# Performance work log

Measured on AMD Instinct MI355X. Metric: run time of the kernel, lower is better.

Reference implementation:

```python
import jax, jax.numpy as jnp
import numpy as np

M, N = 4096, 4096

def _make_expk(n):
    k = np.arange(n, dtype=np.float64) * np.pi / (2.0 * n)
    return jnp.asarray(np.stack([np.cos(k), np.sin(k)], axis=-1), dtype=jnp.float32)

def setup_inputs() -> dict:
    key = jax.random.key(0)
    x = jax.random.normal(key, (M, N), dtype=jnp.float32)
    return {"x": x, "expkM": _make_expk(M), "expkN": _make_expk(N)}

def _idct_last(X, expk):
    """1D IDCT (inverse of unnormalized DCT-II) along last axis via Makhoul's
    N-point FFT trick. expk[k] = (cos, sin) of pi*k/(2N), i.e. e^{j pi k/(2N)}."""
    n = X.shape[-1]
    Xv = X * 0.5
    # V[k] = (Xv[k] - j*Xv[n-k]) * e^{j pi k/(2n)}, with imag part 0 at k=0
    tail = -jnp.flip(Xv, axis=-1)[..., :-1]
    Vi = jnp.concatenate([jnp.zeros_like(Xv[..., :1]), tail], axis=-1)
    W = expk[:, 0] + 1j * expk[:, 1]
    V = (Xv + 1j * Vi) * W
    v = jnp.fft.ifft(V, axis=-1).real.astype(X.dtype)
    # de-interleave: out[2m] = v[m], out[2m+1] = v[n-1-m]
    out = jnp.zeros_like(X)
    out = out.at[..., 0::2].set(v[..., : n - n // 2])
    out = out.at[..., 1::2].set(jnp.flip(v, axis=-1)[..., : n // 2])
    return out

def reference(x, expkM, expkN):
    # separable 2D IDCT: last axis (N) then first axis (M)
    y = _idct_last(x, expkN)
    y = _idct_last(y.T, expkM).T
    return y
```

## Files before the change

### kernel.cpp

```cpp
#include <hip/hip_runtime.h>
#include <math.h>


#define TT 256

constexpr float W64R[32] = {
    1.0f, 0.995184726672197f, 0.980785280403230f, 0.956940335732209f,
    0.923879532511287f, 0.881921264348355f, 0.831469612302545f, 0.773010453362737f,
    0.707106781186548f, 0.634393284163645f, 0.555570233019602f, 0.471396736825998f,
    0.382683432365090f, 0.290284677254462f, 0.195090322016128f, 0.0980171403295606f,
    0.0f, -0.0980171403295606f, -0.195090322016128f, -0.290284677254462f,
    -0.382683432365090f, -0.471396736825998f, -0.555570233019602f, -0.634393284163645f,
    -0.707106781186548f, -0.773010453362737f, -0.831469612302545f, -0.881921264348355f,
    -0.923879532511287f, -0.956940335732209f, -0.980785280403230f, -0.995184726672197f};
constexpr float W64I[32] = {
    0.0f, 0.0980171403295606f, 0.195090322016128f, 0.290284677254462f,
    0.382683432365090f, 0.471396736825998f, 0.555570233019602f, 0.634393284163645f,
    0.707106781186548f, 0.773010453362737f, 0.831469612302545f, 0.881921264348355f,
    0.923879532511287f, 0.956940335732209f, 0.980785280403230f, 0.995184726672197f,
    1.0f, 0.995184726672197f, 0.980785280403230f, 0.956940335732209f,
    0.923879532511287f, 0.881921264348355f, 0.831469612302545f, 0.773010453362737f,
    0.707106781186548f, 0.634393284163645f, 0.555570233019602f, 0.471396736825998f,
    0.382683432365090f, 0.290284677254462f, 0.195090322016128f, 0.0980171403295606f};

__device__ __forceinline__ constexpr int brev(int x, int bits) {
    int r = 0;
    for (int i = 0; i < bits; ++i) { r = (r << 1) | (x & 1); x >>= 1; }
    return r;
}

__device__ __forceinline__ float vadd(float a, float b) { return a + b; }
__device__ __forceinline__ float vsub(float a, float b) { return a - b; }
__device__ __forceinline__ float vmul(float a, float s) { return a * s; }

template <int NP, typename V>
__device__ __forceinline__ void fft_dif(V* re, V* im) {
#pragma unroll
    for (int h = NP / 2; h >= 1; h >>= 1) {
#pragma unroll
        for (int b = 0; b < NP; b += 2 * h) {
#pragma unroll
            for (int k = 0; k < h; ++k) {
                V ur = re[b + k], ui = im[b + k];
                V vr = re[b + k + h], vi = im[b + k + h];
                V dr = vsub(ur, vr), di = vsub(ui, vi);
                re[b + k] = vadd(ur, vr);
                im[b + k] = vadd(ui, vi);
                float wr = W64R[k * (32 / h)], wi = W64I[k * (32 / h)];
                re[b + k + h] = vsub(vmul(dr, wr), vmul(di, wi));
                im[b + k + h] = vadd(vmul(dr, wi), vmul(di, wr));
            }
        }
    }
}

__global__ void tw_init_kernel(float2* __restrict__ tw2048,
                               float2* __restrict__ ca, float2* __restrict__ cb,
                               float2* __restrict__ cc, float2* __restrict__ cd,
                               float4* __restrict__ cAC) {
    int k = blockIdx.x * TT + threadIdx.x;
    const double s = 0.5 / 4096.0;
    double aw = M_PI * (double)k / 2048.0;
    double wr = cos(aw), wi = sin(aw);
    double a1 = M_PI * (double)k / 8192.0;
    double e1r = cos(a1), e1i = sin(a1);
    double a2 = M_PI * (double)(k + 2048) / 8192.0;
    double e2r = cos(a2), e2i = sin(a2);
    double Ar = s * ((1.0 - wi) * e1r - wr * e1i);
    double Ai = s * ((1.0 - wi) * e1i + wr * e1r);
    double Br = (k == 0) ? 0.0 : Ai;
    double Bi = (k == 0) ? 0.0 : -Ar;
    double Cr = s * ((1.0 + wi) * e2r + wr * e2i);
    double Ci = s * ((1.0 + wi) * e2i - wr * e2r);
    ca[k] = make_float2((float)Ar, (float)Ai);
    cb[k] = make_float2((float)Br, (float)Bi);
    cc[k] = make_float2((float)Cr, (float)Ci);
    cd[k] = make_float2((float)Ci, (float)-Cr);
    cAC[k] = make_float4((float)Ar, (float)Ai, (float)Cr, (float)Ci);
    double at = M_PI * (double)k / 1024.0;
    tw2048[k] = make_float2((float)cos(at), (float)sin(at));
}

__global__ __launch_bounds__(TT) void col_a_kernel(
    const float* __restrict__ x, const float4* __restrict__ cAC,
    const float2* __restrict__ tw2048, float2* __restrict__ T1) {
    const int l = threadIdx.x;
    const int par = l >> 5;
    const int c = blockIdx.x * 32 + (l & 31);
    const int k1 = blockIdx.y * 4 + threadIdx.y;
    float fr[16], fi[16];
#pragma unroll
    for (int a = 0; a < 16; ++a) {
        int k2 = 2 * a + par;
        int k = k1 + 64 * k2;
        float xa = x[(size_t)k * 4096 + c];
        float xb = x[(size_t)((4096 - k) & 4095) * 4096 + c];
        float xc = x[(size_t)(2048 + k) * 4096 + c];
        float xd = x[(size_t)(2048 - k) * 4096 + c];
        float4 P = cAC[k];
        float bs = (k == 0) ? 0.0f : 1.0f;
        fr[a] = P.x * xa + bs * P.y * xb + P.z * xc + P.w * xd;
        fi[a] = P.y * xa - bs * P.x * xb + P.w * xc - P.z * xd;
    }
    fft_dif<16, float>(fr, fi);
    const float sgn = par ? -1.0f : 1.0f;
#pragma unroll
    for (int j = 0; j < 16; ++j) {
        int n = brev(j, 4);
        float wr = par ? W64R[2 * n] : 1.0f;
        float wi = par ? W64I[2 * n] : 0.0f;
        float vr = fr[j] * wr - fi[j] * wi;
        float vi = fr[j] * wi + fi[j] * wr;
        float orr = __shfl_xor(vr, 32, 64);
        float oii = __shfl_xor(vi, 32, 64);
        float zr = orr + sgn * vr;
        float zi = oii + sgn * vi;
        int n2 = par ? (n + 16) : n;
        float2 w2 = tw2048[k1 * n2];
        float2 o = make_float2(zr * w2.x - zi * w2.y,
                               zr * w2.y + zi * w2.x);
        T1[(size_t)(k1 * 32 + n2) * 4096 + c] = o;
    }
}

__global__ __launch_bounds__(TT, 1) void col_b_kernel(
    const float2* __restrict__ T1, float* __restrict__ out) {
    const int t = threadIdx.x;
    const int wv = t >> 6;
    const int l = t & 63;
    const int par = l >> 5;
    const int c = blockIdx.x * 32 + (l & 31);
    const int n2 = blockIdx.y * 4 + wv;
    float fr[32], fi[32];
#pragma unroll
    for (int a = 0; a < 32; ++a) {
        int k1 = 2 * a + par;
        float2 v = T1[(size_t)(k1 * 32 + n2) * 4096 + c];
        fr[a] = v.x; fi[a] = v.y;
    }
    fft_dif<32, float>(fr, fi);
    const float sgn = par ? -1.0f : 1.0f;
#pragma unroll
    for (int j = 0; j < 32; ++j) {
        int n = brev(j, 5);
        float wr = par ? W64R[n] : 1.0f;
        float wi = par ? W64I[n] : 0.0f;
        float vr = fr[j] * wr - fi[j] * wi;
        float vi = fr[j] * wi + fi[j] * wr;
        float orr = __shfl_xor(vr, 32, 64);
        float oii = __shfl_xor(vi, 32, 64);
        float zr = orr + sgn * vr;
        float zi = oii + sgn * vi;
        int n1 = par ? (n + 32) : n;
        int m = 32 * n1 + n2;
        int r_re = (n1 < 32) ? 4 * m     : 8191 - 4 * m;
        int r_im = (n1 < 32) ? 4 * m + 2 : 8189 - 4 * m;
        out[(size_t)r_re * 4096 + c] = zr;
        out[(size_t)r_im * 4096 + c] = zi;
    }
}

#define C_SQ2 0.70710678118654752440f
__device__ __forceinline__ void radix8(const float* ar, const float* ai,
                                       float* tr, float* ti) {
    float s04r = ar[0] + ar[4], s04i = ai[0] + ai[4];
    float d04r = ar[0] - ar[4], d04i = ai[0] - ai[4];
    float s26r = ar[2] + ar[6], s26i = ai[2] + ai[6];
    float d26r = ar[2] - ar[6], d26i = ai[2] - ai[6];
    float E0r = s04r + s26r, E0i = s04i + s26i;
    float E1r = d04r - d26i, E1i = d04i + d26r;
    float E2r = s04r - s26r, E2i = s04i - s26i;
    float E3r = d04r + d26i, E3i = d04i - d26r;
    float s15r = ar[1] + ar[5], s15i = ai[1] + ai[5];
    float d15r = ar[1] - ar[5], d15i = ai[1] - ai[5];
    float s37r = ar[3] + ar[7], s37i = ai[3] + ai[7];
    float d37r = ar[3] - ar[7], d37i = ai[3] - ai[7];
    float O0r = s15r + s37r, O0i = s15i + s37i;
    float O1r = d15r - d37i, O1i = d15i + d37r;
    float O2r = s15r - s37r, O2i = s15i - s37i;
    float O3r = d15r + d37i, O3i = d15i - d37r;
    float W1r = C_SQ2 * (O1r - O1i), W1i = C_SQ2 * (O1r + O1i);
    float W2r = -O2i, W2i = O2r;
    float W3r = -C_SQ2 * (O3r + O3i), W3i = C_SQ2 * (O3r - O3i);
    tr[0] = E0r + O0r; ti[0] = E0i + O0i;
    tr[4] = E0r - O0r; ti[4] = E0i - O0i;
    tr[1] = E1r + W1r; ti[1] = E1i + W1i;
    tr[5] = E1r - W1r; ti[5] = E1i - W1i;
    tr[2] = E2r + W2r; ti[2] = E2i + W2i;
    tr[6] = E2r - W2r; ti[6] = E2i - W2i;
    tr[3] = E3r + W3r; ti[3] = E3i + W3i;
    tr[7] = E3r - W3r; ti[7] = E3i - W3i;
}

__global__ __launch_bounds__(TT) void idct_rows_kernel(
    const float2* __restrict__ ca, const float2* __restrict__ cb,
    const float2* __restrict__ cc, const float2* __restrict__ cd,
    const float2* __restrict__ tw2048, float* __restrict__ io) {
    __shared__ float pool[8576];
    float* b0r = pool;
    float* b0i = pool + 2112;
    float* b1r = pool + 4224;
    float* b1i = pool + 6400;
    float* stg = pool + 4224;
    const int t = threadIdx.x;
    float* __restrict__ xr = io + (size_t)blockIdx.x * 4096;

#pragma unroll
    for (int u = 0; u < 4; ++u) {
        int idx = t + 256 * u;
        float4 v = ((const float4*)xr)[idx];
        *(float4*)&stg[4 * idx] = v;
    }
    __syncthreads();

    float zr[8], zi[8], tr[8], ti[8];
#pragma unroll
    for (int p = 0; p < 8; ++p) {
        int k = t + 256 * p;
        float xa = stg[k];
        float xb = stg[(4096 - k) & 4095];
        float xc = stg[2048 + k];
        float xd = stg[2048 - k];
        float2 A = ca[k], B = cb[k], C = cc[k], D = cd[k];
        zr[p] = A.x * xa + B.x * xb + C.x * xc + D.x * xd;
        zi[p] = A.y * xa + B.y * xb + C.y * xc + D.y * xd;
    }
    radix8(zr, zi, tr, ti);
    {
        int baseA = 8 * t + (t >> 2);
        b0r[baseA] = tr[0]; b0i[baseA] = ti[0];
#pragma unroll
        for (int q = 1; q < 8; ++q) {
            float2 w = tw2048[(t * q) & 2047];
            b0r[baseA + q] = w.x * tr[q] - w.y * ti[q];
            b0i[baseA + q] = w.x * ti[q] + w.y * tr[q];
        }
    }
    __syncthreads();
    {
        float ar[8], ai[8];
        int rb = t + (t >> 5);
#pragma unroll
        for (int p = 0; p < 8; ++p) { ar[p] = b0r[rb + 264 * p]; ai[p] = b0i[rb + 264 * p]; }
        radix8(ar, ai, tr, ti);
        int j = t >> 3, k = t & 7, wj = 8 * j;
        int baseB = 68 * j + k;
        b1r[baseB] = tr[0]; b1i[baseB] = ti[0];
#pragma unroll
        for (int q = 1; q < 8; ++q) {
            int off = baseB + 8 * q + (q >> 1);
            float2 w = tw2048[(wj * q) & 2047];
            b1r[off] = w.x * tr[q] - w.y * ti[q];
            b1i[off] = w.x * ti[q] + w.y * tr[q];
        }
    }
    __syncthreads();
    {
        float ar[8], ai[8];
        int rb = t + (t >> 4);
#pragma unroll
        for (int p = 0; p < 8; ++p) { ar[p] = b1r[rb + 272 * p]; ai[p] = b1i[rb + 272 * p]; }
        radix8(ar, ai, tr, ti);
        int j = t >> 6, wj = 64 * j, k = t & 63;
        int baseC = 528 * j + k + (k >> 5);
        b0r[baseC] = tr[0]; b0i[baseC] = ti[0];
#pragma unroll
        for (int q = 1; q < 8; ++q) {
            int off = baseC + 66 * q;
            float2 w = tw2048[(wj * q) & 2047];
            b0r[off] = w.x * tr[q] - w.y * ti[q];
            b0i[off] = w.x * ti[q] + w.y * tr[q];
        }
    }
    __syncthreads();
#pragma unroll
    for (int u = 0; u < 2; ++u) {
        int b = t + 256 * u;
        int rb = b + (b >> 5);
        int wb = b + (b >> 4);
        float a0r = b0r[rb], a0i = b0i[rb];
        float a1r = b0r[rb + 528], a1i = b0i[rb + 528];
        float a2r = b0r[rb + 1056], a2i = b0i[rb + 1056];
        float a3r = b0r[rb + 1584], a3i = b0i[rb + 1584];
        float s02r = a0r + a2r, s02i = a0i + a2i;
        float d02r = a0r - a2r, d02i = a0i - a2i;
        float s13r = a1r + a3r, s13i = a1i + a3i;
        float d13r = a1r - a3r, d13i = a1i - a3i;
        b1r[wb] = s02r + s13r;          b1i[wb] = s02i + s13i;
        b1r[wb + 544] = d02r - d13i;    b1i[wb + 544] = d02i + d13r;
        b1r[wb + 1088] = s02r - s13r;   b1i[wb + 1088] = s02i - s13i;
        b1r[wb + 1632] = d02r + d13i;   b1i[wb + 1632] = d02i - d13r;
    }
    __syncthreads();
#pragma unroll
    for (int i = 0; i < 4; ++i) {
        int s = t + 256 * i;
        int l2 = 2047 - s;
        int ms = s + (s >> 4);
        int ml = l2 + (l2 >> 4);
        float4 o = make_float4(b1r[ms], b1i[ml], b1i[ms], b1r[ml]);
        *(float4*)&xr[4 * s] = o;
    }
}

extern "C" void kernel_launch(void* const* d_in, const int* in_sizes, int n_in,
                              void* d_out, int out_size, void* d_ws, size_t ws_size,
                              hipStream_t stream) {
    const float* x = (const float*)d_in[0];
    float* out = (float*)d_out;

    float2* tw2048 = (float2*)d_ws;
    float2* ca = (float2*)((char*)d_ws + 1 * 16384);
    float2* cb = (float2*)((char*)d_ws + 2 * 16384);
    float2* cc = (float2*)((char*)d_ws + 3 * 16384);
    float2* cd = (float2*)((char*)d_ws + 4 * 16384);
    float4* cAC = (float4*)((char*)d_ws + 5 * 16384);
    float2* T1 = (float2*)((char*)d_ws + (1 << 20));

    tw_init_kernel<<<8, TT, 0, stream>>>(tw2048, ca, cb, cc, cd, cAC);
    col_a_kernel<<<dim3(128, 16), dim3(64, 4), 0, stream>>>(x, cAC, tw2048, T1);
    col_b_kernel<<<dim3(128, 8), TT, 0, stream>>>(T1, out);
    idct_rows_kernel<<<4096, TT, 0, stream>>>(ca, cb, cc, cd, tw2048, out);
}
```

Measured before the change: 188.4 us.

## Stage column-pass input through LDS with direct global-to-LDS 16-byte loads

```diff
diff --git a/kernel.cpp b/kernel.cpp
--- a/kernel.cpp
+++ b/kernel.cpp
@@ -81,27 +81,54 @@
     tw2048[k] = make_float2((float)cos(at), (float)sin(at));
 }
 
-__global__ __launch_bounds__(TT) void col_a_kernel(
+typedef __attribute__((address_space(1))) const unsigned int* ga_u32;
+typedef __attribute__((address_space(3))) unsigned int* la_u32;
+
+__global__ __launch_bounds__(128) void col_a_kernel(
     const float* __restrict__ x, const float4* __restrict__ cAC,
     const float2* __restrict__ tw2048, float2* __restrict__ T1) {
+    __shared__ float L[2][4096];
     const int l = threadIdx.x;
+    const int ty = threadIdx.y;
     const int par = l >> 5;
-    const int c = blockIdx.x * 32 + (l & 31);
-    const int k1 = blockIdx.y * 4 + threadIdx.y;
+    const int cb = blockIdx.x * 32;
+    const int c = cb + (l & 31);
+    const int k1 = blockIdx.y * 2 + ty;
+
+    const int rg = l >> 3;
+    const int cq = (l & 7) * 4;
+#pragma unroll
+    for (int i = 0; i < 16; ++i) {
+        int j = 8 * i + rg;
+        int k2 = j >> 2, s = j & 3;
+        int kk = k1 + 64 * k2;
+        int row = (s == 0) ? kk
+                : (s == 1) ? ((4096 - kk) & 4095)
+                : (s == 2) ? (2048 + kk)
+                           : (2048 - kk);
+        __builtin_amdgcn_global_load_lds(
+            (ga_u32)(const void*)(x + (size_t)row * 4096 + cb + cq),
+            (la_u32)(void*)&L[ty][i * 256 + 4 * l], 16, 0, 0);
+    }
+    __builtin_amdgcn_sched_barrier(0);
+    asm volatile("s_waitcnt vmcnt(0)" ::: "memory");
+    __builtin_amdgcn_sched_barrier(0);
+
     float fr[16], fi[16];
 #pragma unroll
     for (int a = 0; a < 16; ++a) {
-        int k2 = 2 * a + par;
-        int k = k1 + 64 * k2;
-        float xa = x[(size_t)k * 4096 + c];
-        float xb = x[(size_t)((4096 - k) & 4095) * 4096 + c];
-        float xc = x[(size_t)(2048 + k) * 4096 + c];
-        float xd = x[(size_t)(2048 - k) * 4096 + c];
+        int base = (8 * a + 4 * par) * 32 + (l & 31);
+        float xa = L[ty][base];
+        float xb = L[ty][base + 32];
+        float xc = L[ty][base + 64];
+        float xd = L[ty][base + 96];
+        int k = k1 + 64 * (2 * a + par);
         float4 P = cAC[k];
         float bs = (k == 0) ? 0.0f : 1.0f;
         fr[a] = P.x * xa + bs * P.y * xb + P.z * xc + P.w * xd;
         fi[a] = P.y * xa - bs * P.x * xb + P.w * xc - P.z * xd;
     }
+
     fft_dif<16, float>(fr, fi);
     const float sgn = par ? -1.0f : 1.0f;
 #pragma unroll
@@ -318,7 +345,7 @@
     float2* T1 = (float2*)((char*)d_ws + (1 << 20));
 
     tw_init_kernel<<<8, TT, 0, stream>>>(tw2048, ca, cb, cc, cd, cAC);
-    col_a_kernel<<<dim3(128, 16), dim3(64, 4), 0, stream>>>(x, cAC, tw2048, T1);
+    col_a_kernel<<<dim3(128, 32), dim3(64, 2), 0, stream>>>(x, cAC, tw2048, T1);
     col_b_kernel<<<dim3(128, 8), TT, 0, stream>>>(T1, out);
     idct_rows_kernel<<<4096, TT, 0, stream>>>(ca, cb, cc, cd, tw2048, out);
 }
```

After: 190.3 us. No clear change (+1.0%).

## Fuse all IDCT stages into one persistent cooperative kernel with grid syncs

Applied to the files above, without the earlier changes.

```diff
diff --git a/kernel.cpp b/kernel.cpp
--- a/kernel.cpp
+++ b/kernel.cpp
@@ -1,5 +1,8 @@
 #include <hip/hip_runtime.h>
+#include <hip/hip_cooperative_groups.h>
 #include <math.h>
+
+namespace cg = cooperative_groups;
 
 
 #define TT 256
@@ -29,134 +32,24 @@
     return r;
 }
 
-__device__ __forceinline__ float vadd(float a, float b) { return a + b; }
-__device__ __forceinline__ float vsub(float a, float b) { return a - b; }
-__device__ __forceinline__ float vmul(float a, float s) { return a * s; }
-
-template <int NP, typename V>
-__device__ __forceinline__ void fft_dif(V* re, V* im) {
+template <int NP>
+__device__ __forceinline__ void fft_dif(float* re, float* im) {
 #pragma unroll
     for (int h = NP / 2; h >= 1; h >>= 1) {
 #pragma unroll
         for (int b = 0; b < NP; b += 2 * h) {
 #pragma unroll
             for (int k = 0; k < h; ++k) {
-                V ur = re[b + k], ui = im[b + k];
-                V vr = re[b + k + h], vi = im[b + k + h];
-                V dr = vsub(ur, vr), di = vsub(ui, vi);
-                re[b + k] = vadd(ur, vr);
-                im[b + k] = vadd(ui, vi);
+                float ur = re[b + k], ui = im[b + k];
+                float vr = re[b + k + h], vi = im[b + k + h];
+                float dr = ur - vr, di = ui - vi;
+                re[b + k] = ur + vr;
+                im[b + k] = ui + vi;
                 float wr = W64R[k * (32 / h)], wi = W64I[k * (32 / h)];
-                re[b + k + h] = vsub(vmul(dr, wr), vmul(di, wi));
-                im[b + k + h] = vadd(vmul(dr, wi), vmul(di, wr));
-            }
-        }
-    }
-}
-
-__global__ void tw_init_kernel(float2* __restrict__ tw2048,
-                               float2* __restrict__ ca, float2* __restrict__ cb,
-                               float2* __restrict__ cc, float2* __restrict__ cd,
-                               float4* __restrict__ cAC) {
-    int k = blockIdx.x * TT + threadIdx.x;
-    const double s = 0.5 / 4096.0;
-    double aw = M_PI * (double)k / 2048.0;
-    double wr = cos(aw), wi = sin(aw);
-    double a1 = M_PI * (double)k / 8192.0;
-    double e1r = cos(a1), e1i = sin(a1);
-    double a2 = M_PI * (double)(k + 2048) / 8192.0;
-    double e2r = cos(a2), e2i = sin(a2);
-    double Ar = s * ((1.0 - wi) * e1r - wr * e1i);
-    double Ai = s * ((1.0 - wi) * e1i + wr * e1r);
-    double Br = (k == 0) ? 0.0 : Ai;
-    double Bi = (k == 0) ? 0.0 : -Ar;
-    double Cr = s * ((1.0 + wi) * e2r + wr * e2i);
-    double Ci = s * ((1.0 + wi) * e2i - wr * e2r);
-    ca[k] = make_float2((float)Ar, (float)Ai);
-    cb[k] = make_float2((float)Br, (float)Bi);
-    cc[k] = make_float2((float)Cr, (float)Ci);
-    cd[k] = make_float2((float)Ci, (float)-Cr);
-    cAC[k] = make_float4((float)Ar, (float)Ai, (float)Cr, (float)Ci);
-    double at = M_PI * (double)k / 1024.0;
-    tw2048[k] = make_float2((float)cos(at), (float)sin(at));
-}
-
-__global__ __launch_bounds__(TT) void col_a_kernel(
-    const float* __restrict__ x, const float4* __restrict__ cAC,
-    const float2* __restrict__ tw2048, float2* __restrict__ T1) {
-    const int l = threadIdx.x;
-    const int par = l >> 5;
-    const int c = blockIdx.x * 32 + (l & 31);
-    const int k1 = blockIdx.y * 4 + threadIdx.y;
-    float fr[16], fi[16];
-#pragma unroll
-    for (int a = 0; a < 16; ++a) {
-        int k2 = 2 * a + par;
-        int k = k1 + 64 * k2;
-        float xa = x[(size_t)k * 4096 + c];
-        float xb = x[(size_t)((4096 - k) & 4095) * 4096 + c];
-        float xc = x[(size_t)(2048 + k) * 4096 + c];
-        float xd = x[(size_t)(2048 - k) * 4096 + c];
-        float4 P = cAC[k];
-        float bs = (k == 0) ? 0.0f : 1.0f;
-        fr[a] = P.x * xa + bs * P.y * xb + P.z * xc + P.w * xd;
-        fi[a] = P.y * xa - bs * P.x * xb + P.w * xc - P.z * xd;
-    }
-    fft_dif<16, float>(fr, fi);
-    const float sgn = par ? -1.0f : 1.0f;
-#pragma unroll
-    for (int j = 0; j < 16; ++j) {
-        int n = brev(j, 4);
-        float wr = par ? W64R[2 * n] : 1.0f;
-        float wi = par ? W64I[2 * n] : 0.0f;
-        float vr = fr[j] * wr - fi[j] * wi;
-        float vi = fr[j] * wi + fi[j] * wr;
-        float orr = __shfl_xor(vr, 32, 64);
-        float oii = __shfl_xor(vi, 32, 64);
-        float zr = orr + sgn * vr;
-        float zi = oii + sgn * vi;
-        int n2 = par ? (n + 16) : n;
-        float2 w2 = tw2048[k1 * n2];
-        float2 o = make_float2(zr * w2.x - zi * w2.y,
-                               zr * w2.y + zi * w2.x);
-        T1[(size_t)(k1 * 32 + n2) * 4096 + c] = o;
-    }
-}
-
-__global__ __launch_bounds__(TT, 1) void col_b_kernel(
-    const float2* __restrict__ T1, float* __restrict__ out) {
-    const int t = threadIdx.x;
-    const int wv = t >> 6;
-    const int l = t & 63;
-    const int par = l >> 5;
-    const int c = blockIdx.x * 32 + (l & 31);
-    const int n2 = blockIdx.y * 4 + wv;
-    float fr[32], fi[32];
-#pragma unroll
-    for (int a = 0; a < 32; ++a) {
-        int k1 = 2 * a + par;
-        float2 v = T1[(size_t)(k1 * 32 + n2) * 4096 + c];
-        fr[a] = v.x; fi[a] = v.y;
-    }
-    fft_dif<32, float>(fr, fi);
-    const float sgn = par ? -1.0f : 1.0f;
-#pragma unroll
-    for (int j = 0; j < 32; ++j) {
-        int n = brev(j, 5);
-        float wr = par ? W64R[n] : 1.0f;
-        float wi = par ? W64I[n] : 0.0f;
-        float vr = fr[j] * wr - fi[j] * wi;
-        float vi = fr[j] * wi + fi[j] * wr;
-        float orr = __shfl_xor(vr, 32, 64);
-        float oii = __shfl_xor(vi, 32, 64);
-        float zr = orr + sgn * vr;
-        float zi = oii + sgn * vi;
-        int n1 = par ? (n + 32) : n;
-        int m = 32 * n1 + n2;
-        int r_re = (n1 < 32) ? 4 * m     : 8191 - 4 * m;
-        int r_im = (n1 < 32) ? 4 * m + 2 : 8189 - 4 * m;
-        out[(size_t)r_re * 4096 + c] = zr;
-        out[(size_t)r_im * 4096 + c] = zi;
+                re[b + k + h] = dr * wr - di * wi;
+                im[b + k + h] = dr * wi + di * wr;
+            }
+        }
     }
 }
 
@@ -192,114 +85,228 @@
     tr[7] = E3r - W3r; ti[7] = E3i - W3i;
 }
 
-__global__ __launch_bounds__(TT) void idct_rows_kernel(
-    const float2* __restrict__ ca, const float2* __restrict__ cb,
-    const float2* __restrict__ cc, const float2* __restrict__ cd,
-    const float2* __restrict__ tw2048, float* __restrict__ io) {
+__global__ __launch_bounds__(TT, 4) void idct2_fused(
+    const float* __restrict__ x,
+    float2* __restrict__ tw2048,
+    float2* __restrict__ ca, float2* __restrict__ cb,
+    float2* __restrict__ cc, float2* __restrict__ cd,
+    float4* __restrict__ cAC,
+    float2* __restrict__ T1, float* __restrict__ out) {
+    cg::grid_group grid = cg::this_grid();
+    const int t = threadIdx.x;
+    const int bid = blockIdx.x;
+    const int gdim = gridDim.x;
     __shared__ float pool[8576];
-    float* b0r = pool;
-    float* b0i = pool + 2112;
-    float* b1r = pool + 4224;
-    float* b1i = pool + 6400;
-    float* stg = pool + 4224;
-    const int t = threadIdx.x;
-    float* __restrict__ xr = io + (size_t)blockIdx.x * 4096;
-
-#pragma unroll
-    for (int u = 0; u < 4; ++u) {
-        int idx = t + 256 * u;
-        float4 v = ((const float4*)xr)[idx];
-        *(float4*)&stg[4 * idx] = v;
-    }
-    __syncthreads();
-
-    float zr[8], zi[8], tr[8], ti[8];
-#pragma unroll
-    for (int p = 0; p < 8; ++p) {
-        int k = t + 256 * p;
-        float xa = stg[k];
-        float xb = stg[(4096 - k) & 4095];
-        float xc = stg[2048 + k];
-        float xd = stg[2048 - k];
-        float2 A = ca[k], B = cb[k], C = cc[k], D = cd[k];
-        zr[p] = A.x * xa + B.x * xb + C.x * xc + D.x * xd;
-        zi[p] = A.y * xa + B.y * xb + C.y * xc + D.y * xd;
-    }
-    radix8(zr, zi, tr, ti);
+
+    if (bid < 8) {
+        int k = bid * TT + t;
+        const double s = 0.5 / 4096.0;
+        double aw = M_PI * (double)k / 2048.0;
+        double wr = cos(aw), wi = sin(aw);
+        double a1 = M_PI * (double)k / 8192.0;
+        double e1r = cos(a1), e1i = sin(a1);
+        double a2 = M_PI * (double)(k + 2048) / 8192.0;
+        double e2r = cos(a2), e2i = sin(a2);
+        double Ar = s * ((1.0 - wi) * e1r - wr * e1i);
+        double Ai = s * ((1.0 - wi) * e1i + wr * e1r);
+        double Br = (k == 0) ? 0.0 : Ai;
+        double Bi = (k == 0) ? 0.0 : -Ar;
+        double Cr = s * ((1.0 + wi) * e2r + wr * e2i);
+        double Ci = s * ((1.0 + wi) * e2i - wr * e2r);
+        ca[k] = make_float2((float)Ar, (float)Ai);
+        cb[k] = make_float2((float)Br, (float)Bi);
+        cc[k] = make_float2((float)Cr, (float)Ci);
+        cd[k] = make_float2((float)Ci, (float)-Cr);
+        cAC[k] = make_float4((float)Ar, (float)Ai, (float)Cr, (float)Ci);
+        double at = M_PI * (double)k / 1024.0;
+        tw2048[k] = make_float2((float)cos(at), (float)sin(at));
+    }
+    grid.sync();
+
+    for (int vb = bid; vb < 2048; vb += gdim) {
+        const int bx = vb & 127, by = vb >> 7;
+        const int l = t & 63;
+        const int ty = t >> 6;
+        const int par = l >> 5;
+        const int c = bx * 32 + (l & 31);
+        const int k1 = by * 4 + ty;
+        float fr[16], fi[16];
+#pragma unroll
+        for (int a = 0; a < 16; ++a) {
+            int k = k1 + 64 * (2 * a + par);
+            float xa = x[(size_t)k * 4096 + c];
+            float xb = x[(size_t)((4096 - k) & 4095) * 4096 + c];
+            float xc = x[(size_t)(2048 + k) * 4096 + c];
+            float xd = x[(size_t)(2048 - k) * 4096 + c];
+            float4 P = cAC[k];
+            float bs = (k == 0) ? 0.0f : 1.0f;
+            fr[a] = P.x * xa + bs * P.y * xb + P.z * xc + P.w * xd;
+            fi[a] = P.y * xa - bs * P.x * xb + P.w * xc - P.z * xd;
+        }
+        fft_dif<16>(fr, fi);
+        const float sgn = par ? -1.0f : 1.0f;
+#pragma unroll
+        for (int j = 0; j < 16; ++j) {
+            int n = brev(j, 4);
+            float wr = par ? W64R[2 * n] : 1.0f;
+            float wi = par ? W64I[2 * n] : 0.0f;
+            float vr = fr[j] * wr - fi[j] * wi;
+            float vi = fr[j] * wi + fi[j] * wr;
+            float orr = __shfl_xor(vr, 32, 64);
+            float oii = __shfl_xor(vi, 32, 64);
+            float zr = orr + sgn * vr;
+            float zi = oii + sgn * vi;
+            int n2 = par ? (n + 16) : n;
+            float2 w2 = tw2048[k1 * n2];
+            float2 o = make_float2(zr * w2.x - zi * w2.y,
+                                   zr * w2.y + zi * w2.x);
+            T1[(size_t)(k1 * 32 + n2) * 4096 + c] = o;
+        }
+    }
+    grid.sync();
+
+    for (int vb = bid; vb < 1024; vb += gdim) {
+        const int bx = vb & 127, by = vb >> 7;
+        const int wv = t >> 6;
+        const int l = t & 63;
+        const int par = l >> 5;
+        const int c = bx * 32 + (l & 31);
+        const int n2 = by * 4 + wv;
+        float fr[32], fi[32];
+#pragma unroll
+        for (int a = 0; a < 32; ++a) {
+            int k1 = 2 * a + par;
+            float2 v = T1[(size_t)(k1 * 32 + n2) * 4096 + c];
+            fr[a] = v.x; fi[a] = v.y;
+        }
+        fft_dif<32>(fr, fi);
+        const float sgn = par ? -1.0f : 1.0f;
+#pragma unroll
+        for (int j = 0; j < 32; ++j) {
+            int n = brev(j, 5);
+            float wr = par ? W64R[n] : 1.0f;
+            float wi = par ? W64I[n] : 0.0f;
+            float vr = fr[j] * wr - fi[j] * wi;
+            float vi = fr[j] * wi + fi[j] * wr;
+            float orr = __shfl_xor(vr, 32, 64);
+            float oii = __shfl_xor(vi, 32, 64);
+            float zr = orr + sgn * vr;
+            float zi = oii + sgn * vi;
+            int n1 = par ? (n + 32) : n;
+            int m = 32 * n1 + n2;
+            int r_re = (n1 < 32) ? 4 * m     : 8191 - 4 * m;
+            int r_im = (n1 < 32) ? 4 * m + 2 : 8189 - 4 * m;
+            out[(size_t)r_re * 4096 + c] = zr;
+            out[(size_t)r_im * 4096 + c] = zi;
+        }
+    }
+    grid.sync();
+
     {
-        int baseA = 8 * t + (t >> 2);
-        b0r[baseA] = tr[0]; b0i[baseA] = ti[0];
-#pragma unroll
-        for (int q = 1; q < 8; ++q) {
-            float2 w = tw2048[(t * q) & 2047];
-            b0r[baseA + q] = w.x * tr[q] - w.y * ti[q];
-            b0i[baseA + q] = w.x * ti[q] + w.y * tr[q];
-        }
-    }
-    __syncthreads();
-    {
-        float ar[8], ai[8];
-        int rb = t + (t >> 5);
-#pragma unroll
-        for (int p = 0; p < 8; ++p) { ar[p] = b0r[rb + 264 * p]; ai[p] = b0i[rb + 264 * p]; }
-        radix8(ar, ai, tr, ti);
-        int j = t >> 3, k = t & 7, wj = 8 * j;
-        int baseB = 68 * j + k;
-        b1r[baseB] = tr[0]; b1i[baseB] = ti[0];
-#pragma unroll
-        for (int q = 1; q < 8; ++q) {
-            int off = baseB + 8 * q + (q >> 1);
-            float2 w = tw2048[(wj * q) & 2047];
-            b1r[off] = w.x * tr[q] - w.y * ti[q];
-            b1i[off] = w.x * ti[q] + w.y * tr[q];
-        }
-    }
-    __syncthreads();
-    {
-        float ar[8], ai[8];
-        int rb = t + (t >> 4);
-#pragma unroll
-        for (int p = 0; p < 8; ++p) { ar[p] = b1r[rb + 272 * p]; ai[p] = b1i[rb + 272 * p]; }
-        radix8(ar, ai, tr, ti);
-        int j = t >> 6, wj = 64 * j, k = t & 63;
-        int baseC = 528 * j + k + (k >> 5);
-        b0r[baseC] = tr[0]; b0i[baseC] = ti[0];
-#pragma unroll
-        for (int q = 1; q < 8; ++q) {
-            int off = baseC + 66 * q;
-            float2 w = tw2048[(wj * q) & 2047];
-            b0r[off] = w.x * tr[q] - w.y * ti[q];
-            b0i[off] = w.x * ti[q] + w.y * tr[q];
-        }
-    }
-    __syncthreads();
-#pragma unroll
-    for (int u = 0; u < 2; ++u) {
-        int b = t + 256 * u;
-        int rb = b + (b >> 5);
-        int wb = b + (b >> 4);
-        float a0r = b0r[rb], a0i = b0i[rb];
-        float a1r = b0r[rb + 528], a1i = b0i[rb + 528];
-        float a2r = b0r[rb + 1056], a2i = b0i[rb + 1056];
-        float a3r = b0r[rb + 1584], a3i = b0i[rb + 1584];
-        float s02r = a0r + a2r, s02i = a0i + a2i;
-        float d02r = a0r - a2r, d02i = a0i - a2i;
-        float s13r = a1r + a3r, s13i = a1i + a3i;
-        float d13r = a1r - a3r, d13i = a1i - a3i;
-        b1r[wb] = s02r + s13r;          b1i[wb] = s02i + s13i;
-        b1r[wb + 544] = d02r - d13i;    b1i[wb + 544] = d02i + d13r;
-        b1r[wb + 1088] = s02r - s13r;   b1i[wb + 1088] = s02i - s13i;
-        b1r[wb + 1632] = d02r + d13i;   b1i[wb + 1632] = d02i - d13r;
-    }
-    __syncthreads();
-#pragma unroll
-    for (int i = 0; i < 4; ++i) {
-        int s = t + 256 * i;
-        int l2 = 2047 - s;
-        int ms = s + (s >> 4);
-        int ml = l2 + (l2 >> 4);
-        float4 o = make_float4(b1r[ms], b1i[ml], b1i[ms], b1r[ml]);
-        *(float4*)&xr[4 * s] = o;
+        float* b0r = pool;
+        float* b0i = pool + 2112;
+        float* b1r = pool + 4224;
+        float* b1i = pool + 6400;
+        float* stg = pool + 4224;
+        for (int vb = bid; vb < 4096; vb += gdim) {
+            float* __restrict__ xr = out + (size_t)vb * 4096;
+#pragma unroll
+            for (int u = 0; u < 4; ++u) {
+                int idx = t + 256 * u;
+                float4 v = ((const float4*)xr)[idx];
+                *(float4*)&stg[4 * idx] = v;
+            }
+            __syncthreads();
+            float zr[8], zi[8], tr[8], ti[8];
+#pragma unroll
+            for (int p = 0; p < 8; ++p) {
+                int k = t + 256 * p;
+                float xa = stg[k];
+                float xb = stg[(4096 - k) & 4095];
+                float xc = stg[2048 + k];
+                float xd = stg[2048 - k];
+                float2 A = ca[k], B = cb[k], C = cc[k], D = cd[k];
+                zr[p] = A.x * xa + B.x * xb + C.x * xc + D.x * xd;
+                zi[p] = A.y * xa + B.y * xb + C.y * xc + D.y * xd;
+            }
+            radix8(zr, zi, tr, ti);
+            {
+                int baseA = 8 * t + (t >> 2);
+                b0r[baseA] = tr[0]; b0i[baseA] = ti[0];
+#pragma unroll
+                for (int q = 1; q < 8; ++q) {
+                    float2 w = tw2048[(t * q) & 2047];
+                    b0r[baseA + q] = w.x * tr[q] - w.y * ti[q];
+                    b0i[baseA + q] = w.x * ti[q] + w.y * tr[q];
+                }
+            }
+            __syncthreads();
+            {
+                float ar[8], ai[8];
+                int rb = t + (t >> 5);
+#pragma unroll
+                for (int p = 0; p < 8; ++p) { ar[p] = b0r[rb + 264 * p]; ai[p] = b0i[rb + 264 * p]; }
+                radix8(ar, ai, tr, ti);
+                int j = t >> 3, k = t & 7, wj = 8 * j;
+                int baseB = 68 * j + k;
+                b1r[baseB] = tr[0]; b1i[baseB] = ti[0];
+#pragma unroll
+                for (int q = 1; q < 8; ++q) {
+                    int off = baseB + 8 * q + (q >> 1);
+                    float2 w = tw2048[(wj * q) & 2047];
+                    b1r[off] = w.x * tr[q] - w.y * ti[q];
+                    b1i[off] = w.x * ti[q] + w.y * tr[q];
+                }
+            }
+            __syncthreads();
+            {
+                float ar[8], ai[8];
+                int rb = t + (t >> 4);
+#pragma unroll
+                for (int p = 0; p < 8; ++p) { ar[p] = b1r[rb + 272 * p]; ai[p] = b1i[rb + 272 * p]; }
+                radix8(ar, ai, tr, ti);
+                int j = t >> 6, wj = 64 * j, k = t & 63;
+                int baseC = 528 * j + k + (k >> 5);
+                b0r[baseC] = tr[0]; b0i[baseC] = ti[0];
+#pragma unroll
+                for (int q = 1; q < 8; ++q) {
+                    int off = baseC + 66 * q;
+                    float2 w = tw2048[(wj * q) & 2047];
+                    b0r[off] = w.x * tr[q] - w.y * ti[q];
+                    b0i[off] = w.x * ti[q] + w.y * tr[q];
+                }
+            }
+            __syncthreads();
+#pragma unroll
+            for (int u = 0; u < 2; ++u) {
+                int b = t + 256 * u;
+                int rb = b + (b >> 5);
+                int wb = b + (b >> 4);
+                float a0r = b0r[rb], a0i = b0i[rb];
+                float a1r = b0r[rb + 528], a1i = b0i[rb + 528];
+                float a2r = b0r[rb + 1056], a2i = b0i[rb + 1056];
+                float a3r = b0r[rb + 1584], a3i = b0i[rb + 1584];
+                float s02r = a0r + a2r, s02i = a0i + a2i;
+                float d02r = a0r - a2r, d02i = a0i - a2i;
+                float s13r = a1r + a3r, s13i = a1i + a3i;
+                float d13r = a1r - a3r, d13i = a1i - a3i;
+                b1r[wb] = s02r + s13r;          b1i[wb] = s02i + s13i;
+                b1r[wb + 544] = d02r - d13i;    b1i[wb + 544] = d02i + d13r;
+                b1r[wb + 1088] = s02r - s13r;   b1i[wb + 1088] = s02i - s13i;
+                b1r[wb + 1632] = d02r + d13i;   b1i[wb + 1632] = d02i - d13r;
+            }
+            __syncthreads();
+#pragma unroll
+            for (int i = 0; i < 4; ++i) {
+                int s = t + 256 * i;
+                int l2 = 2047 - s;
+                int ms = s + (s >> 4);
+                int ml = l2 + (l2 >> 4);
+                float4 o = make_float4(b1r[ms], b1i[ml], b1i[ms], b1r[ml]);
+                *(float4*)&xr[4 * s] = o;
+            }
+            __syncthreads();
+        }
     }
 }
 
@@ -317,8 +324,19 @@
     float4* cAC = (float4*)((char*)d_ws + 5 * 16384);
     float2* T1 = (float2*)((char*)d_ws + (1 << 20));
 
-    tw_init_kernel<<<8, TT, 0, stream>>>(tw2048, ca, cb, cc, cd, cAC);
-    col_a_kernel<<<dim3(128, 16), dim3(64, 4), 0, stream>>>(x, cAC, tw2048, T1);
-    col_b_kernel<<<dim3(128, 8), TT, 0, stream>>>(T1, out);
-    idct_rows_kernel<<<4096, TT, 0, stream>>>(ca, cb, cc, cd, tw2048, out);
-}
+    int occ = 0;
+    hipOccupancyMaxActiveBlocksPerMultiprocessor(&occ, idct2_fused, TT, 0);
+    if (occ < 1) occ = 1;
+    int ncu = 0;
+    if (hipDeviceGetAttribute(&ncu, hipDeviceAttributeMultiprocessorCount, 0)
+            != hipSuccess || ncu <= 0)
+        ncu = 256;
+    int blocks = occ * ncu;
+    if (blocks > 1024) blocks = 1024;
+
+    void* args[] = {(void*)&x, (void*)&tw2048, (void*)&ca, (void*)&cb,
+                    (void*)&cc, (void*)&cd, (void*)&cAC, (void*)&T1,
+                    (void*)&out};
+    hipLaunchCooperativeKernel(idct2_fused, dim3(blocks), dim3(TT),
+                               args, 0, stream);
+}
```

After: 509.9 us. 171% more time.
